# Optimization experiments

Measured on AMD Instinct MI355X. Metric: run time of the kernel, lower is better.

Reference implementation:

```python
import jax, jax.numpy as jnp
import numpy as np

N, E = 100000, 1600000
NODE_IN, EDGE_IN, H = 128, 16, 128


def sage_conv(x, src, dst, Wl, Wr, b, n_nodes):
    # PyG SAGEConv (aggr='mean'): out = lin_l(mean_{j->i} x_j) + lin_r(x_i), bias on lin_l
    msg_sum = jax.ops.segment_sum(x[src], dst, num_segments=n_nodes)      # [N, d]
    cnt = jax.ops.segment_sum(jnp.ones((src.shape[0],), x.dtype), dst, num_segments=n_nodes)
    mean = msg_sum / jnp.maximum(cnt, 1.0)[:, None]                        # empty neighborhoods -> 0
    return mean @ Wl + x @ Wr + b


def setup_inputs() -> dict:
    key = jax.random.key(0)
    ks = jax.random.split(key, 12)
    s = lambda d: 1.0 / np.sqrt(d)
    return {
        "x": jax.random.normal(ks[0], (N, NODE_IN), jnp.float32),
        "edge_index": jax.random.randint(ks[1], (2, E), 0, N, dtype=jnp.int64),
        "edge_attr": jax.random.normal(ks[2], (E, EDGE_IN), jnp.float32),
        "Wl1": jax.random.normal(ks[3], (NODE_IN, H), jnp.float32) * s(NODE_IN),
        "Wr1": jax.random.normal(ks[4], (NODE_IN, H), jnp.float32) * s(NODE_IN),
        "b1": jnp.zeros((H,), jnp.float32),
        "Wl2": jax.random.normal(ks[5], (H, H), jnp.float32) * s(H),
        "Wr2": jax.random.normal(ks[6], (H, H), jnp.float32) * s(H),
        "b2": jnp.zeros((H,), jnp.float32),
        "Wm1": jax.random.normal(ks[7], (2 * H + EDGE_IN, H), jnp.float32) * s(2 * H + EDGE_IN),
        "bm1": jnp.zeros((H,), jnp.float32),
        "Wm2": jax.random.normal(ks[8], (H, 1), jnp.float32) * s(H),
        "bm2": jnp.zeros((1,), jnp.float32),
    }


def reference(x, edge_index, edge_attr, Wl1, Wr1, b1, Wl2, Wr2, b2, Wm1, bm1, Wm2, bm2):
    src, dst = edge_index[0], edge_index[1]
    h = jax.nn.relu(sage_conv(x, src, dst, Wl1, Wr1, b1, N))
    h = jax.nn.relu(sage_conv(h, src, dst, Wl2, Wr2, b2, N))
    edge_feat = jnp.concatenate([h[src], h[dst], edge_attr], axis=1)  # [E, 2H+edge_in]
    out = jax.nn.relu(edge_feat @ Wm1 + bm1) @ Wm2 + bm2               # dropout is identity in eval
    return out.reshape(-1)
```

## Files before the change

### kernel.cpp

```cpp
#include <hip/hip_runtime.h>

typedef _Float16 f16;
typedef _Float16 f16x8 __attribute__((ext_vector_type(8)));
typedef float f32x4 __attribute__((ext_vector_type(4)));

#define MFMA16(a,b,c) __builtin_amdgcn_mfma_f32_16x16x32_f16((a),(b),(c),0,0,0)

__global__ void k_detect(const long long* ei, int n_nodes, int* flag) {
    if (blockIdx.x == 0 && threadIdx.x == 0) {
        int ok = 1;
        for (int i = 0; i < 64; i++) {
            long long v = ei[i];
            if (v < 0 || v >= n_nodes) { ok = 0; break; }
        }
        *flag = ok;
    }
}

__global__ void k_idx(const void* ei, int E, const int* __restrict__ flag,
                      int* __restrict__ src, int* __restrict__ dst) {
    int e = blockIdx.x * 256 + threadIdx.x;
    if (e >= E) return;
    if (*flag) {
        const long long* p = (const long long*)ei;
        src[e] = (int)p[e];
        dst[e] = (int)p[(size_t)E + e];
    } else {
        const int* p = (const int*)ei;
        src[e] = p[e];
        dst[e] = p[(size_t)E + e];
    }
}

__global__ void k_x2h(const float* __restrict__ x, f16* __restrict__ xh, int n) {
    int i = (blockIdx.x * 256 + threadIdx.x) * 8;
    if (i >= n) return;
    float4 a = *(const float4*)(x + i);
    float4 b = *(const float4*)(x + i + 4);
    f16x8 h;
    h[0] = (f16)a.x; h[1] = (f16)a.y; h[2] = (f16)a.z; h[3] = (f16)a.w;
    h[4] = (f16)b.x; h[5] = (f16)b.y; h[6] = (f16)b.z; h[7] = (f16)b.w;
    *(f16x8*)(xh + i) = h;
}

__global__ void k_wfrag(const float* __restrict__ Wa, const float* __restrict__ Wb,
                        f16* __restrict__ dst, int KS) {
    int t = blockIdx.x * 256 + threadIdx.x;
    int total = KS * 8 * 64;
    if (t >= total) return;
    int l = t & 63;
    int s = t >> 9;
    int k0 = s * 32 + (l >> 4) * 8;
    int j = ((t >> 6) & 7) * 16 + (l & 15);
    f16x8 h;
    #pragma unroll
    for (int e = 0; e < 8; e++) {
        int k = k0 + e;
        float v = (k < 128) ? Wa[k * 128 + j] : Wb[(k - 128) * 128 + j];
        h[e] = (f16)v;
    }
    *(f16x8*)(dst + (size_t)t * 8) = h;
}

__global__ void k_zfrag(const float* __restrict__ Wm1, f16* __restrict__ dst) {
    int t = blockIdx.x * 256 + threadIdx.x;
    if (t >= 4 * 16 * 64) return;
    int lane = t & 63, c = (t >> 6) & 15, s = t >> 10;
    int k0 = s * 32 + (lane >> 4) * 8;
    int j = c * 16 + (lane & 15);
    f16x8 h;
    #pragma unroll
    for (int e = 0; e < 8; e++) {
        int k = k0 + e;
        float v = (j < 128) ? Wm1[k * 128 + j] : Wm1[(128 + k) * 128 + (j - 128)];
        h[e] = (f16)v;
    }
    *(f16x8*)(dst + (size_t)t * 8) = h;
}

__global__ void k_wefrag(const float* __restrict__ Wm1, f16* __restrict__ dst) {
    int t = blockIdx.x * 256 + threadIdx.x;
    if (t >= 8 * 64) return;
    int lane = t & 63, ct = t >> 6;
    int k0 = (lane >> 4) * 8;
    int j = ct * 16 + (lane & 15);
    f16x8 h;
    #pragma unroll
    for (int e = 0; e < 8; e++) {
        int k = k0 + e;
        h[e] = (k < 16) ? (f16)Wm1[(256 + k) * 128 + j] : (f16)0.0f;
    }
    *(f16x8*)(dst + (size_t)t * 8) = h;
}

__global__ void k_hist(const int* __restrict__ dst, int E, int* __restrict__ deg) {
    int e = blockIdx.x * 256 + threadIdx.x;
    if (e < E) atomicAdd(&deg[dst[e]], 1);
}

__global__ void k_bsum(const int* __restrict__ deg, int n, int* __restrict__ bsum) {
    __shared__ int ws[4];
    const int tid = threadIdx.x;
    int i = blockIdx.x * 1024 + tid * 4;
    int s = 0;
    if (i + 3 < n) {
        int4 d = *(const int4*)(deg + i);
        s = d.x + d.y + d.z + d.w;
    } else {
        #pragma unroll
        for (int j = 0; j < 4; j++) if (i + j < n) s += deg[i + j];
    }
    #pragma unroll
    for (int m = 1; m < 64; m <<= 1) s += __shfl_xor(s, m, 64);
    if ((tid & 63) == 0) ws[tid >> 6] = s;
    __syncthreads();
    if (tid == 0) bsum[blockIdx.x] = ws[0] + ws[1] + ws[2] + ws[3];
}

__global__ void k_bscan(int* __restrict__ bsum, int nb, int* __restrict__ rowptr_n) {
    __shared__ int wsum[4];
    const int tid = threadIdx.x, lane = tid & 63, wid = tid >> 6;
    int v = (tid < nb) ? bsum[tid] : 0;
    int inc = v;
    #pragma unroll
    for (int off = 1; off < 64; off <<= 1) {
        int u = __shfl_up(inc, off, 64);
        if (lane >= off) inc += u;
    }
    if (lane == 63) wsum[wid] = inc;
    __syncthreads();
    int woff = 0;
    for (int j = 0; j < wid; j++) woff += wsum[j];
    int excl = woff + inc - v;
    if (tid < nb) bsum[tid] = excl;
    if (tid == nb - 1) rowptr_n[0] = excl + v;
}

__global__ void k_rowptr(const int* __restrict__ deg, int n, const int* __restrict__ boff,
                         int* __restrict__ rowptr, int* __restrict__ cursor) {
    __shared__ int wsum[4];
    const int tid = threadIdx.x, lane = tid & 63, wid = tid >> 6;
    int i = blockIdx.x * 1024 + tid * 4;
    int d0 = 0, d1 = 0, d2 = 0, d3 = 0;
    if (i + 3 < n) {
        int4 d = *(const int4*)(deg + i);
        d0 = d.x; d1 = d.y; d2 = d.z; d3 = d.w;
    } else {
        if (i     < n) d0 = deg[i];
        if (i + 1 < n) d1 = deg[i + 1];
        if (i + 2 < n) d2 = deg[i + 2];
        if (i + 3 < n) d3 = deg[i + 3];
    }
    int s = d0 + d1 + d2 + d3;
    int inc = s;
    #pragma unroll
    for (int off = 1; off < 64; off <<= 1) {
        int u = __shfl_up(inc, off, 64);
        if (lane >= off) inc += u;
    }
    if (lane == 63) wsum[wid] = inc;
    __syncthreads();
    int woff = 0;
    for (int j = 0; j < wid; j++) woff += wsum[j];
    int excl = boff[blockIdx.x] + woff + inc - s;
    int e1 = excl + d0, e2 = e1 + d1, e3 = e2 + d2;
    if (i     < n) { rowptr[i]     = excl; cursor[i]     = excl; }
    if (i + 1 < n) { rowptr[i + 1] = e1;   cursor[i + 1] = e1; }
    if (i + 2 < n) { rowptr[i + 2] = e2;   cursor[i + 2] = e2; }
    if (i + 3 < n) { rowptr[i + 3] = e3;   cursor[i + 3] = e3; }
}

__global__ void k_scatter(const int* __restrict__ src, const int* __restrict__ dst, int E,
                          int* __restrict__ cursor, int* __restrict__ col) {
    int e = blockIdx.x * 256 + threadIdx.x;
    if (e < E) {
        int p = atomicAdd(&cursor[dst[e]], 1);
        col[p] = src[e];
    }
}

__global__ __launch_bounds__(256) void k_agg(
    const f16* __restrict__ tab, const int* __restrict__ rowptr,
    const int* __restrict__ col, f16* __restrict__ mean, int n_nodes) {
    const int gw = (int)((blockIdx.x * (unsigned)blockDim.x + threadIdx.x) >> 6);
    const int lane = threadIdx.x & 63;
    if (gw >= n_nodes) return;
    const int g = lane >> 4, c = lane & 15;
    const int s0 = rowptr[gw], s1 = rowptr[gw + 1];
    float acc[8] = {0.f, 0.f, 0.f, 0.f, 0.f, 0.f, 0.f, 0.f};
    int k = s0 + g;
    for (; k + 4 < s1; k += 8) {
        const int n0 = col[k], n1 = col[k + 4];
        f16x8 v0 = *(const f16x8*)(tab + (size_t)n0 * 128 + c * 8);
        f16x8 v1 = *(const f16x8*)(tab + (size_t)n1 * 128 + c * 8);
        #pragma unroll
        for (int j = 0; j < 8; j++) acc[j] += (float)v0[j] + (float)v1[j];
    }
    if (k < s1) {
        const int n0 = col[k];
        f16x8 v0 = *(const f16x8*)(tab + (size_t)n0 * 128 + c * 8);
        #pragma unroll
        for (int j = 0; j < 8; j++) acc[j] += (float)v0[j];
    }
    #pragma unroll
    for (int j = 0; j < 8; j++) {
        acc[j] += __shfl_xor(acc[j], 16, 64);
        acc[j] += __shfl_xor(acc[j], 32, 64);
    }
    int d = s1 - s0; if (d < 1) d = 1;
    const float inv = 1.f / (float)d;
    if (g == 0) {
        f16x8 r;
        #pragma unroll
        for (int j = 0; j < 8; j++) r[j] = (f16)(acc[j] * inv);
        *(f16x8*)(mean + (size_t)gw * 128 + c * 8) = r;
    }
}

__global__ __launch_bounds__(256, 2) void k_gemm_sage(
    const f16* __restrict__ A1, const f16* __restrict__ A2,
    const f16* __restrict__ Wf, const float* __restrict__ bias,
    f16* __restrict__ out, int n_rows, int iters, int gridW) {
    __shared__ __align__(16) f16 sW[8 * 8 * 64 * 8];
    const int tid = threadIdx.x, lane = tid & 63, w = tid >> 6;
    const int l15 = lane & 15, g = lane >> 4;
    for (int i = tid; i < 8 * 8 * 64; i += 256)
        *(uint4*)&sW[(size_t)i * 8] = *(const uint4*)&Wf[(size_t)i * 8];
    __syncthreads();
    const int c0 = (2 * w) * 16 + l15, c1 = (2 * w + 1) * 16 + l15;
    const float b0 = bias[c0], b1 = bias[c1];
    for (int it = 0; it < iters; ++it) {
        const int base = (blockIdx.x + it * gridW) * 64;
        if (base >= n_rows) break;
        f32x4 acc[4][2];
        #pragma unroll
        for (int t = 0; t < 4; t++) {
            acc[t][0] = f32x4{b0, b0, b0, b0};
            acc[t][1] = f32x4{b1, b1, b1, b1};
        }
        #pragma unroll
        for (int s = 0; s < 8; s++) {
            const f16* Asrc = (s < 4) ? A1 : A2;
            const int koff = (s & 3) * 32 + g * 8;
            f16x8 bf0 = *(const f16x8*)&sW[((s * 8 + 2 * w    ) * 64 + lane) * 8];
            f16x8 bf1 = *(const f16x8*)&sW[((s * 8 + 2 * w + 1) * 64 + lane) * 8];
            #pragma unroll
            for (int t = 0; t < 4; t++) {
                int row = base + t * 16 + l15;
                if (row >= n_rows) row = n_rows - 1;
                f16x8 a = *(const f16x8*)(Asrc + (size_t)row * 128 + koff);
                acc[t][0] = MFMA16(a, bf0, acc[t][0]);
                acc[t][1] = MFMA16(a, bf1, acc[t][1]);
            }
        }
        #pragma unroll
        for (int t = 0; t < 4; t++) {
            #pragma unroll
            for (int i = 0; i < 4; i++) {
                int row = base + t * 16 + g * 4 + i;
                if (row < n_rows) {
                    float v0 = acc[t][0][i]; v0 = v0 > 0.f ? v0 : 0.f;
                    float v1 = acc[t][1][i]; v1 = v1 > 0.f ? v1 : 0.f;
                    out[(size_t)row * 128 + c0] = (f16)v0;
                    out[(size_t)row * 128 + c1] = (f16)v1;
                }
            }
        }
    }
}

__global__ __launch_bounds__(256, 2) void k_zgemm(
    const f16* __restrict__ h2, const f16* __restrict__ zwf,
    const float* __restrict__ bm1, f16* __restrict__ z,
    int n_rows, int iters, int gridW) {
    const int tid = threadIdx.x, lane = tid & 63, w = tid >> 6;
    const int l15 = lane & 15, g = lane >> 4;
    f16x8 wf[4][4];
    #pragma unroll
    for (int s = 0; s < 4; s++)
        #pragma unroll
        for (int cc = 0; cc < 4; cc++)
            wf[s][cc] = *(const f16x8*)(zwf + ((size_t)((s * 16 + 4 * w + cc) * 64 + lane)) * 8);
    float bias[4];
    #pragma unroll
    for (int cc = 0; cc < 4; cc++) {
        int j = (4 * w + cc) * 16 + l15;
        bias[cc] = (j >= 128) ? bm1[j - 128] : 0.0f;
    }
    for (int it = 0; it < iters; ++it) {
        const int base = (blockIdx.x + it * gridW) * 64;
        if (base >= n_rows) break;
        f32x4 acc[4][4];
        #pragma unroll
        for (int t = 0; t < 4; t++)
            #pragma unroll
            for (int cc = 0; cc < 4; cc++)
                acc[t][cc] = f32x4{bias[cc], bias[cc], bias[cc], bias[cc]};
        #pragma unroll
        for (int s = 0; s < 4; s++) {
            f16x8 a[4];
            #pragma unroll
            for (int t = 0; t < 4; t++) {
                int row = base + t * 16 + l15;
                if (row >= n_rows) row = n_rows - 1;
                a[t] = *(const f16x8*)(h2 + (size_t)row * 128 + s * 32 + g * 8);
            }
            #pragma unroll
            for (int cc = 0; cc < 4; cc++)
                #pragma unroll
                for (int t = 0; t < 4; t++)
                    acc[t][cc] = MFMA16(a[t], wf[s][cc], acc[t][cc]);
        }
        #pragma unroll
        for (int t = 0; t < 4; t++)
            #pragma unroll
            for (int cc = 0; cc < 4; cc++)
                #pragma unroll
                for (int i = 0; i < 4; i++) {
                    int row = base + t * 16 + g * 4 + i;
                    if (row < n_rows)
                        z[(size_t)row * 256 + (4 * w + cc) * 16 + l15] = (f16)acc[t][cc][i];
                }
    }
}

#define ZP 136
__global__ __launch_bounds__(256, 4) void k_edge2(
    const f16* __restrict__ z, const float* __restrict__ ea,
    const int* __restrict__ src, const int* __restrict__ dst,
    const f16* __restrict__ wef, const float* __restrict__ Wm2,
    const float* __restrict__ bm2, float* __restrict__ out,
    int E, int iters, int gridW) {
    __shared__ __align__(16) f16 sZ[64 * ZP];
    __shared__ __align__(16) f16 sEA[4 * 64 * 8];
    __shared__ float sPart[4][64];
    const int tid = threadIdx.x, lane = tid & 63, w = tid >> 6;
    const int l15 = lane & 15, g = lane >> 4;
    const int sr = lane >> 2, sq = lane & 3;
    const int slot_s = w * 16 + sr;

    for (int i = tid; i < 4 * 64; i += 256)
        *(f16x8*)(&sEA[0] + (size_t)i * 8) = f16x8{};

    const f16x8 be0 = *(const f16x8*)(wef + ((size_t)((2 * w) * 64 + lane)) * 8);
    const f16x8 be1 = *(const f16x8*)(wef + ((size_t)((2 * w + 1) * 64 + lane)) * 8);
    const float w20 = Wm2[(2 * w) * 16 + l15];
    const float w21 = Wm2[(2 * w + 1) * 16 + l15];
    const float bv = bm2[0];

    f16x8 zs[4], zd[4];
    union { f16 h[4]; uint2 u2; } eh;

    auto stage_load = [&](int ebase) {
        int er = ebase + slot_s; if (er > E - 1) er = E - 1;
        const int is = src[er], id = dst[er];
        const f16* ps = z + (size_t)is * 256 + sq * 32;
        const f16* pd = z + (size_t)id * 256 + 128 + sq * 32;
        #pragma unroll
        for (int i = 0; i < 4; i++) {
            zs[i] = *(const f16x8*)(ps + i * 8);
            zd[i] = *(const f16x8*)(pd + i * 8);
        }
        float4 ev = *(const float4*)(ea + (size_t)er * 16 + sq * 4);
        eh.h[0] = (f16)ev.x; eh.h[1] = (f16)ev.y; eh.h[2] = (f16)ev.z; eh.h[3] = (f16)ev.w;
    };
    auto stage_write = [&]() {
        f16* zp = &sZ[0] + slot_s * ZP + sq * 32;
        #pragma unroll
        for (int i = 0; i < 4; i++) {
            f16x8 v = zs[i] + zd[i];
            *(f16x8*)(zp + i * 8) = v;
        }
        f16* ep = &sEA[0] +
                  ((size_t)((slot_s >> 4) * 64 + (sq >> 1) * 16 + (slot_s & 15)) * 8 + (sq & 1) * 4);
        *(uint2*)ep = eh.u2;
    };

    stage_load(blockIdx.x * 64);
    __syncthreads();
    stage_write();
    __syncthreads();

    for (int it = 0; it < iters; ++it) {
        const int ebase = (blockIdx.x + it * gridW) * 64;
        if (ebase >= E) break;
        const int nxt = (blockIdx.x + (it + 1) * gridW) * 64;
        const bool has_next = (it + 1 < iters) && (nxt < E);
        if (has_next) stage_load(nxt);

        f32x4 acc[4][2];
        #pragma unroll
        for (int t = 0; t < 4; t++) { acc[t][0] = f32x4{0,0,0,0}; acc[t][1] = f32x4{0,0,0,0}; }
        #pragma unroll
        for (int t = 0; t < 4; t++) {
            f16x8 a = *(const f16x8*)(&sEA[0] + ((size_t)(t * 64 + lane)) * 8);
            acc[t][0] = MFMA16(a, be0, acc[t][0]);
            acc[t][1] = MFMA16(a, be1, acc[t][1]);
        }
        #pragma unroll
        for (int t = 0; t < 4; t++) {
            float p[4];
            #pragma unroll
            for (int i = 0; i < 4; i++) {
                int slot = t * 16 + g * 4 + i;
                float z0 = (float)sZ[slot * ZP + (2 * w) * 16 + l15];
                float z1 = (float)sZ[slot * ZP + (2 * w + 1) * 16 + l15];
                float v0 = z0 + acc[t][0][i]; v0 = v0 > 0.f ? v0 : 0.f;
                float v1 = z1 + acc[t][1][i]; v1 = v1 > 0.f ? v1 : 0.f;
                p[i] = v0 * w20 + v1 * w21;
            }
            #pragma unroll
            for (int m = 1; m < 16; m <<= 1)
                #pragma unroll
                for (int i = 0; i < 4; i++) p[i] += __shfl_xor(p[i], m, 64);
            if (l15 == 0)
                #pragma unroll
                for (int i = 0; i < 4; i++) sPart[w][t * 16 + g * 4 + i] = p[i];
        }
        __syncthreads();
        if (tid < 64) {
            int e = ebase + tid;
            if (e < E)
                out[e] = sPart[0][tid] + sPart[1][tid] + sPart[2][tid] + sPart[3][tid] + bv;
        }
        if (has_next) stage_write();
        __syncthreads();
    }
}

extern "C" void kernel_launch(void* const* d_in, const int* in_sizes, int n_in,
                              void* d_out, int out_size, void* d_ws, size_t ws_size,
                              hipStream_t stream) {
    const float* x   = (const float*)d_in[0];
    const void*  ei  = d_in[1];
    const float* ea  = (const float*)d_in[2];
    const float* Wl1 = (const float*)d_in[3];
    const float* Wr1 = (const float*)d_in[4];
    const float* b1  = (const float*)d_in[5];
    const float* Wl2 = (const float*)d_in[6];
    const float* Wr2 = (const float*)d_in[7];
    const float* b2  = (const float*)d_in[8];
    const float* Wm1 = (const float*)d_in[9];
    const float* bm1 = (const float*)d_in[10];
    const float* Wm2 = (const float*)d_in[11];
    const float* bm2 = (const float*)d_in[12];

    const int N = in_sizes[0] / 128;
    const int E = in_sizes[1] / 2;

    char* ws = (char*)d_ws;
    size_t off = 0;
    auto alloc = [&](size_t bytes) -> void* {
        void* p = ws + off;
        off = (off + bytes + 255) & ~(size_t)255;
        return p;
    };
    f16* xh     = (f16*)alloc((size_t)N * 128 * 2);
    f16* mean   = (f16*)alloc((size_t)N * 128 * 2);
    f16* h1     = (f16*)alloc((size_t)N * 128 * 2);
    int* src    = (int*)alloc((size_t)E * 4);
    int* dst    = (int*)alloc((size_t)E * 4);
    int* col    = (int*)alloc((size_t)E * 4);
    int* deg    = (int*)alloc((size_t)N * 4);
    int* rowptr = (int*)alloc((size_t)(N + 1) * 4);
    int* cursor = (int*)alloc((size_t)N * 4);
    int* bsum   = (int*)alloc((size_t)1024 * 4);
    f16* w1f    = (f16*)alloc((size_t)8 * 8 * 64 * 8 * 2);
    f16* w2f    = (f16*)alloc((size_t)8 * 8 * 64 * 8 * 2);
    f16* zwf    = (f16*)alloc((size_t)4 * 16 * 64 * 8 * 2);
    f16* wef    = (f16*)alloc((size_t)8 * 64 * 8 * 2);
    int* flag   = (int*)alloc(4);
    if (off > ws_size) return;
    f16* h2 = xh;
    f16* z  = mean;

    const int eb = (E + 255) / 256;
    const int nbk = (N + 1023) / 1024;

    k_detect<<<1, 64, 0, stream>>>((const long long*)ei, N, flag);
    k_idx<<<eb, 256, 0, stream>>>(ei, E, flag, src, dst);
    k_x2h<<<(N * 128 / 8 + 255) / 256, 256, 0, stream>>>(x, xh, N * 128);
    k_wfrag<<<16, 256, 0, stream>>>(Wl1, Wr1, w1f, 8);
    k_wfrag<<<16, 256, 0, stream>>>(Wl2, Wr2, w2f, 8);
    k_zfrag<<<16, 256, 0, stream>>>(Wm1, zwf);
    k_wefrag<<<2, 256, 0, stream>>>(Wm1, wef);

    hipMemsetAsync(deg, 0, (size_t)N * 4, stream);
    k_hist<<<eb, 256, 0, stream>>>(dst, E, deg);
    k_bsum<<<nbk, 256, 0, stream>>>(deg, N, bsum);
    k_bscan<<<1, 256, 0, stream>>>(bsum, nbk, rowptr + N);
    k_rowptr<<<nbk, 256, 0, stream>>>(deg, N, bsum, rowptr, cursor);
    k_scatter<<<eb, 256, 0, stream>>>(src, dst, E, cursor, col);

    const int gridW = 512;
    const int rb = (N + 63) / 64;
    const int g_iters = (rb + gridW - 1) / gridW;

    k_agg<<<(N + 3) / 4, 256, 0, stream>>>(xh, rowptr, col, mean, N);
    k_gemm_sage<<<gridW, 256, 0, stream>>>(mean, xh, w1f, b1, h1, N, g_iters, gridW);
    k_agg<<<(N + 3) / 4, 256, 0, stream>>>(h1, rowptr, col, mean, N);
    k_gemm_sage<<<gridW, 256, 0, stream>>>(mean, h1, w2f, b2, h2, N, g_iters, gridW);

    const int zg = 512;
    const int z_iters = (rb + zg - 1) / zg;
    k_zgemm<<<zg, 256, 0, stream>>>(h2, zwf, bm1, z, N, z_iters, zg);

    const int eg = 1280;
    const int nb = (E + 63) / 64;
    const int e_iters = (nb + eg - 1) / eg;
    k_edge2<<<eg, 256, 0, stream>>>(z, ea, src, dst, wef, Wm2, bm2,
                                    (float*)d_out, E, e_iters, eg);
}
```

Measured before the change: 602.8 us.

## Process edges in dst-sorted CSR order in edge MLP, widen aggregation unroll

The edge MLP kernel now walks edges in CSR (destination-sorted) order, using new eid and dstp arrays filled during the scatter step. Consecutive edges then share destination rows of z, which improves cache reuse for the dst half of the gather, while edge_attr reads and output writes become scattered through eid. The aggregation loop is unrolled to four neighbors per step, occupancy hint and grid size of the edge kernel are raised, and the detect kernel uses a wave ballot instead of a serial loop. The scatter step now does two extra stores per edge.

```diff
diff --git a/kernel.cpp b/kernel.cpp
--- a/kernel.cpp
+++ b/kernel.cpp
@@ -7,14 +7,10 @@
 #define MFMA16(a,b,c) __builtin_amdgcn_mfma_f32_16x16x32_f16((a),(b),(c),0,0,0)
 
 __global__ void k_detect(const long long* ei, int n_nodes, int* flag) {
-    if (blockIdx.x == 0 && threadIdx.x == 0) {
-        int ok = 1;
-        for (int i = 0; i < 64; i++) {
-            long long v = ei[i];
-            if (v < 0 || v >= n_nodes) { ok = 0; break; }
-        }
-        *flag = ok;
-    }
+    long long v = ei[threadIdx.x];
+    int bad = (v < 0 || v >= n_nodes);
+    unsigned long long m = __ballot(bad);
+    if (threadIdx.x == 0) *flag = (m == 0ULL);
 }
 
 __global__ void k_idx(const void* ei, int E, const int* __restrict__ flag,
@@ -171,11 +167,15 @@
 }
 
 __global__ void k_scatter(const int* __restrict__ src, const int* __restrict__ dst, int E,
-                          int* __restrict__ cursor, int* __restrict__ col) {
+                          int* __restrict__ cursor, int* __restrict__ col,
+                          int* __restrict__ eid, int* __restrict__ dstp) {
     int e = blockIdx.x * 256 + threadIdx.x;
     if (e < E) {
-        int p = atomicAdd(&cursor[dst[e]], 1);
+        int d = dst[e];
+        int p = atomicAdd(&cursor[d], 1);
         col[p] = src[e];
+        eid[p] = e;
+        dstp[p] = d;
     }
 }
 
@@ -189,14 +189,17 @@
     const int s0 = rowptr[gw], s1 = rowptr[gw + 1];
     float acc[8] = {0.f, 0.f, 0.f, 0.f, 0.f, 0.f, 0.f, 0.f};
     int k = s0 + g;
-    for (; k + 4 < s1; k += 8) {
-        const int n0 = col[k], n1 = col[k + 4];
+    for (; k + 12 < s1; k += 16) {
+        const int n0 = col[k], n1 = col[k + 4], n2 = col[k + 8], n3 = col[k + 12];
         f16x8 v0 = *(const f16x8*)(tab + (size_t)n0 * 128 + c * 8);
         f16x8 v1 = *(const f16x8*)(tab + (size_t)n1 * 128 + c * 8);
-        #pragma unroll
-        for (int j = 0; j < 8; j++) acc[j] += (float)v0[j] + (float)v1[j];
-    }
-    if (k < s1) {
+        f16x8 v2 = *(const f16x8*)(tab + (size_t)n2 * 128 + c * 8);
+        f16x8 v3 = *(const f16x8*)(tab + (size_t)n3 * 128 + c * 8);
+        #pragma unroll
+        for (int j = 0; j < 8; j++)
+            acc[j] += ((float)v0[j] + (float)v1[j]) + ((float)v2[j] + (float)v3[j]);
+    }
+    for (; k < s1; k += 4) {
         const int n0 = col[k];
         f16x8 v0 = *(const f16x8*)(tab + (size_t)n0 * 128 + c * 8);
         #pragma unroll
@@ -325,9 +328,9 @@
 }
 
 #define ZP 136
-__global__ __launch_bounds__(256, 4) void k_edge2(
+__global__ __launch_bounds__(256, 7) void k_edge2(
     const f16* __restrict__ z, const float* __restrict__ ea,
-    const int* __restrict__ src, const int* __restrict__ dst,
+    const int* __restrict__ colp, const int* __restrict__ dstp, const int* __restrict__ eidp,
     const f16* __restrict__ wef, const float* __restrict__ Wm2,
     const float* __restrict__ bm2, float* __restrict__ out,
     int E, int iters, int gridW) {
@@ -351,9 +354,9 @@
     f16x8 zs[4], zd[4];
     union { f16 h[4]; uint2 u2; } eh;
 
-    auto stage_load = [&](int ebase) {
-        int er = ebase + slot_s; if (er > E - 1) er = E - 1;
-        const int is = src[er], id = dst[er];
+    auto stage_load = [&](int pbase) {
+        int pr = pbase + slot_s; if (pr > E - 1) pr = E - 1;
+        const int is = colp[pr], id = dstp[pr], ee = eidp[pr];
         const f16* ps = z + (size_t)is * 256 + sq * 32;
         const f16* pd = z + (size_t)id * 256 + 128 + sq * 32;
         #pragma unroll
@@ -361,7 +364,7 @@
             zs[i] = *(const f16x8*)(ps + i * 8);
             zd[i] = *(const f16x8*)(pd + i * 8);
         }
-        float4 ev = *(const float4*)(ea + (size_t)er * 16 + sq * 4);
+        float4 ev = *(const float4*)(ea + (size_t)ee * 16 + sq * 4);
         eh.h[0] = (f16)ev.x; eh.h[1] = (f16)ev.y; eh.h[2] = (f16)ev.z; eh.h[3] = (f16)ev.w;
     };
     auto stage_write = [&]() {
@@ -382,8 +385,8 @@
     __syncthreads();
 
     for (int it = 0; it < iters; ++it) {
-        const int ebase = (blockIdx.x + it * gridW) * 64;
-        if (ebase >= E) break;
+        const int pbase = (blockIdx.x + it * gridW) * 64;
+        if (pbase >= E) break;
         const int nxt = (blockIdx.x + (it + 1) * gridW) * 64;
         const bool has_next = (it + 1 < iters) && (nxt < E);
         if (has_next) stage_load(nxt);
@@ -419,9 +422,11 @@
         }
         __syncthreads();
         if (tid < 64) {
-            int e = ebase + tid;
-            if (e < E)
+            int p = pbase + tid;
+            if (p < E) {
+                int e = eidp[p];
                 out[e] = sPart[0][tid] + sPart[1][tid] + sPart[2][tid] + sPart[3][tid] + bv;
+            }
         }
         if (has_next) stage_write();
         __syncthreads();
@@ -461,6 +466,8 @@
     int* src    = (int*)alloc((size_t)E * 4);
     int* dst    = (int*)alloc((size_t)E * 4);
     int* col    = (int*)alloc((size_t)E * 4);
+    int* eid    = (int*)alloc((size_t)E * 4);
+    int* dstp   = (int*)alloc((size_t)E * 4);
     int* deg    = (int*)alloc((size_t)N * 4);
     int* rowptr = (int*)alloc((size_t)(N + 1) * 4);
     int* cursor = (int*)alloc((size_t)N * 4);
@@ -490,7 +497,7 @@
     k_bsum<<<nbk, 256, 0, stream>>>(deg, N, bsum);
     k_bscan<<<1, 256, 0, stream>>>(bsum, nbk, rowptr + N);
     k_rowptr<<<nbk, 256, 0, stream>>>(deg, N, bsum, rowptr, cursor);
-    k_scatter<<<eb, 256, 0, stream>>>(src, dst, E, cursor, col);
+    k_scatter<<<eb, 256, 0, stream>>>(src, dst, E, cursor, col, eid, dstp);
 
     const int gridW = 512;
     const int rb = (N + 63) / 64;
@@ -505,9 +512,9 @@
     const int z_iters = (rb + zg - 1) / zg;
     k_zgemm<<<zg, 256, 0, stream>>>(h2, zwf, bm1, z, N, z_iters, zg);
 
-    const int eg = 1280;
+    const int eg = 1792;
     const int nb = (E + 63) / 64;
     const int e_iters = (nb + eg - 1) / eg;
-    k_edge2<<<eg, 256, 0, stream>>>(z, ea, src, dst, wef, Wm2, bm2,
+    k_edge2<<<eg, 256, 0, stream>>>(z, ea, col, dstp, eid, wef, Wm2, bm2,
                                     (float*)d_out, E, e_iters, eg);
 }
```

Result: slower. 810.9 us (+34.5%).
